# Kernel tuning notes

Measured on AMD Instinct MI355X. Metric: run time of the kernel, lower is better.

## Reference

```python
import jax, jax.numpy as jnp
import numpy as np


def setup_inputs() -> dict:
    key = jax.random.key(0)
    kq, kk, kv = jax.random.split(key, 3)
    B, H, T, D = 2, 8, 8192, 64
    return {
        "Q": jax.random.normal(kq, (B, H, T, D), dtype=jnp.float32),
        "K": jax.random.normal(kk, (B, H, T, D), dtype=jnp.float32),
        "V": jax.random.normal(kv, (B, H, T, D), dtype=jnp.float32),
        "window_size": 512,
    }


def _gather_bands(x, nb, Wn):
    # x: [B,H,T,D] -> [B,H,nb,3*Wn,D], key blocks (i-1, i, i+1) per query block i
    B, H, T, D = x.shape
    xb = x.reshape(B, H, nb, Wn, D)
    xp = jnp.pad(xb, ((0, 0), (0, 0), (1, 1), (0, 0), (0, 0)))
    return jnp.concatenate([xp[:, :, i:i + nb] for i in range(3)], axis=3)


def reference(Q, K, V, window_size):
    # Sliding-window attention: softmax over keys with |q_idx - kv_idx| <= window_size,
    # computed block-sparsely (only the 3 neighboring key blocks per query block).
    B, H, T, D = Q.shape
    Wn = int(window_size)
    assert T % Wn == 0
    nb = T // Wn
    scale = 1.0 / (D ** 0.5)

    Qb = Q.reshape(B, H, nb, Wn, D)
    Kw = _gather_bands(K, nb, Wn)  # [B,H,nb,3W,D]
    Vw = _gather_bands(V, nb, Wn)

    # scores within the band: [B,H,nb,W,3W]
    s = jnp.einsum('bhnqd,bhnkd->bhnqk', Qb, Kw) * scale

    # exact band mask: global q = n*W + q_loc, global kv = (n-1)*W + k_loc
    q_loc = jnp.arange(Wn)[:, None]
    k_loc = jnp.arange(3 * Wn)[None, :]
    band = jnp.abs(q_loc + Wn - k_loc) <= Wn          # [W, 3W]
    kv_g = (jnp.arange(nb)[:, None] - 1) * Wn + jnp.arange(3 * Wn)[None, :]  # [nb, 3W]
    valid = (kv_g >= 0) & (kv_g < T)
    mask = band[None, :, :] & valid[:, None, :]        # [nb, W, 3W]

    s = jnp.where(mask[None, None], s, -jnp.inf)
    p = jax.nn.softmax(s, axis=-1)
    o = jnp.einsum('bhnqk,bhnkd->bhnqd', p, Vw)
    return o.reshape(B, H, T, D)
```

## Files before the change

### kernel.cpp

```cpp
#include <hip/hip_runtime.h>
#include <hip/hip_bf16.h>
#include <stdint.h>

typedef __attribute__((ext_vector_type(8))) short bf16x8;
typedef __attribute__((ext_vector_type(4))) short bf16x4;
typedef __attribute__((ext_vector_type(4))) float f32x4;

#define T_SEQ   8192
#define D_HEAD  64
#define NHEADS  16
#define WIN     512
#define BQ      128
#define BK      64
#define NTILES  (T_SEQ / BK)
#define LDSR    72
#define MASKVAL (-1.0e6f)

#define WS_NEEDED ((size_t)2 * NHEADS * T_SEQ * D_HEAD * 2)

#define MFMA16(a,b,c) __builtin_amdgcn_mfma_f32_16x16x16bf16_1k(a,b,c,0,0,0)

extern "C" __device__ __attribute__((const)) float __ocml_native_exp2_f32(float);
__device__ __forceinline__ float fexp2(float x) { return __ocml_native_exp2_f32(x); }

#define GLDS16(g, l) __builtin_amdgcn_global_load_lds( \
    (const __attribute__((address_space(1))) void*)(g), \
    (__attribute__((address_space(3))) void*)(l), 16, 0, 0)

__device__ __forceinline__ short f2bf(float f) {
    union { float f; uint32_t u; } v; v.f = f;
    return (short)((v.u + 0x7FFFu + ((v.u >> 16) & 1u)) >> 16);
}

__device__ __forceinline__ uint32_t pkbf2(float lo, float hi) {
    union { __hip_bfloat162 h; uint32_t u; } c;
    c.h = __float22bfloat162_rn(make_float2(lo, hi));
    return c.u;
}

__global__ __launch_bounds__(256, 2)
void prep_kv(const float* __restrict__ Kg, const float* __restrict__ Vg,
             short* __restrict__ Kb, short* __restrict__ Vt)
{
    __shared__ float vt[64 * 65];
    const int tid  = threadIdx.x;
    const int tile = blockIdx.x & (NTILES - 1);
    const int head = blockIdx.x >> 7;
    const size_t off = ((size_t)head * T_SEQ + (size_t)tile * BK) * D_HEAD;

    const float* ks = Kg + off;
    short* kd = Kb + off;
    #pragma unroll
    for (int i = 0; i < 2; ++i) {
        int L = tid + 256 * i;
        int row = L >> 3, c = L & 7;
        const float* s = ks + row * 64 + c * 8;
        float4 a = *(const float4*)s;
        float4 b = *(const float4*)(s + 4);
        short out[8] = { f2bf(a.x), f2bf(a.y), f2bf(a.z), f2bf(a.w),
                         f2bf(b.x), f2bf(b.y), f2bf(b.z), f2bf(b.w) };
        *(bf16x8*)(kd + (row * 8 + (c ^ (row & 7))) * 8) = *(bf16x8*)out;
    }

    const float* vs = Vg + off;
    #pragma unroll
    for (int i = 0; i < 4; ++i) {
        int idx = tid + 256 * i;
        int row = idx >> 4, c4 = (idx & 15) << 2;
        float4 v = *(const float4*)(vs + row * D_HEAD + c4);
        *(float4*)&vt[row * 65 + c4] = v;
    }
    __syncthreads();
    short* vd = Vt + ((size_t)head * NTILES + tile) * (BK * D_HEAD);
    {
        int d = tid >> 2, q = tid & 3;
        #pragma unroll
        for (int h = 0; h < 2; ++h) {
            int c = h * 4 + q;
            short out[8];
            #pragma unroll
            for (int j = 0; j < 4; ++j) out[j]     = f2bf(vt[(h*32      + q*4 + j) * 65 + d]);
            #pragma unroll
            for (int j = 0; j < 4; ++j) out[4 + j] = f2bf(vt[(h*32 + 16 + q*4 + j) * 65 + d]);
            *(bf16x8*)(vd + (d * 8 + (c ^ (d & 7))) * 8) = *(bf16x8*)out;
        }
    }
}

__global__ __launch_bounds__(256, 4)
void swa_fwd(const float* __restrict__ Qg, const short* __restrict__ Kb,
             const short* __restrict__ Vt, float* __restrict__ Og)
{
    __shared__ short Ks[2][BK * D_HEAD];
    __shared__ short Vs[2][BK * D_HEAD];

    const int tid  = threadIdx.x;
    const int wave = tid >> 6;
    const int lane = tid & 63;
    const int lcol = lane & 15;
    const int quad = lane >> 4;
    const int rx   = lcol & 7;

    const int g    = blockIdx.x;
    const int head = g >> 6;
    const int qt   = ((g & 7) << 3) | ((g >> 3) & 7);
    const int q0   = qt * BQ;
    const int tq   = q0 >> 6;

    const float* Qp = Qg + (size_t)head * T_SEQ * D_HEAD;
    const short* Kp = Kb + (size_t)head * T_SEQ * D_HEAD;
    float*       Op = Og + (size_t)head * T_SEQ * D_HEAD;

    const float qscale = 0.125f * 1.44269504088896340736f;
    const int qrow_w = q0 + wave * 32;

    bf16x8 qf[2][2];
    #pragma unroll
    for (int mt = 0; mt < 2; ++mt) {
        const float* qptr = Qp + (size_t)(qrow_w + mt*16 + lcol) * D_HEAD + quad * 8;
        #pragma unroll
        for (int ks = 0; ks < 2; ++ks) {
            float4 a = *(const float4*)(qptr + ks*32);
            float4 b = *(const float4*)(qptr + ks*32 + 4);
            bf16x8 f;
            f[0]=f2bf(a.x*qscale); f[1]=f2bf(a.y*qscale); f[2]=f2bf(a.z*qscale); f[3]=f2bf(a.w*qscale);
            f[4]=f2bf(b.x*qscale); f[5]=f2bf(b.y*qscale); f[6]=f2bf(b.z*qscale); f[7]=f2bf(b.w*qscale);
            qf[mt][ks] = f;
        }
    }

    f32x4 oacc[2][4];
    f32x4 lacc[2];
    const f32x4 zero4 = {0.f, 0.f, 0.f, 0.f};
    const short oneb = (short)0x3F80;
    const bf16x4 ones4 = {oneb, oneb, oneb, oneb};
    #pragma unroll
    for (int mt = 0; mt < 2; ++mt) {
        lacc[mt] = zero4;
        #pragma unroll
        for (int nt = 0; nt < 4; ++nt) oacc[mt][nt] = zero4;
    }

    int t0 = (q0 - WIN) >> 6;            if (t0 < 0) t0 = 0;
    int t1 = (q0 + BQ - 1 + WIN) >> 6;   if (t1 > NTILES - 1) t1 = NTILES - 1;

    const int ch0 = wave * 2, ch1 = wave * 2 + 1;

    {
        const short* ksrc = Kp + (size_t)t0 * (BK * D_HEAD);
        const short* vsrc = Vt + ((size_t)head * NTILES + t0) * (BK * D_HEAD);
        GLDS16(ksrc + ch0*512 + lane*8, &Ks[0][ch0*512]);
        GLDS16(ksrc + ch1*512 + lane*8, &Ks[0][ch1*512]);
        GLDS16(vsrc + ch0*512 + lane*8, &Vs[0][ch0*512]);
        GLDS16(vsrc + ch1*512 + lane*8, &Vs[0][ch1*512]);
    }
    asm volatile("s_waitcnt vmcnt(0)" ::: "memory");
    __syncthreads();

    auto body = [&](int t, int P) {
        {
            const int tn = (t + 1 <= t1) ? t + 1 : t1;
            const short* ksrc = Kp + (size_t)tn * (BK * D_HEAD);
            const short* vsrc = Vt + ((size_t)head * NTILES + tn) * (BK * D_HEAD);
            short* kds = &Ks[P^1][0];
            short* vds = &Vs[P^1][0];
            GLDS16(ksrc + ch0*512 + lane*8, kds + ch0*512);
            GLDS16(ksrc + ch1*512 + lane*8, kds + ch1*512);
            GLDS16(vsrc + ch0*512 + lane*8, vds + ch0*512);
            GLDS16(vsrc + ch1*512 + lane*8, vds + ch1*512);
        }

        const short* Kcur = &Ks[P][0];
        const short* Vcur = &Vs[P][0];
        const bool edge = (t < tq - 6) || (t > tq + 7);

        #pragma unroll
        for (int h = 0; h < 2; ++h) {
            bf16x8 vv[4];
            #pragma unroll
            for (int nt = 0; nt < 4; ++nt)
                vv[nt] = *(const bf16x8*)&Vcur[(nt*16 + lcol)*64 + (((h*4 + quad) ^ rx) << 3)];

            f32x4 sc[2][2];
            #pragma unroll
            for (int j = 0; j < 2; ++j) { sc[j][0] = zero4; sc[j][1] = zero4; }
            #pragma unroll
            for (int ks = 0; ks < 2; ++ks) {
                #pragma unroll
                for (int j = 0; j < 2; ++j) {
                    bf16x8 kf = *(const bf16x8*)&Kcur[((2*h+j)*16 + lcol)*64
                                                      + (((ks*4 + quad) ^ rx) << 3)];
                    sc[j][0] = __builtin_amdgcn_mfma_f32_16x16x32_bf16(kf, qf[0][ks], sc[j][0], 0,0,0);
                    sc[j][1] = __builtin_amdgcn_mfma_f32_16x16x32_bf16(kf, qf[1][ks], sc[j][1], 0,0,0);
                }
            }

            if (edge) {
                #pragma unroll
                for (int j = 0; j < 2; ++j) {
                    const int kg0 = t*BK + (2*h+j)*16 + quad*4;
                    #pragma unroll
                    for (int mt = 0; mt < 2; ++mt) {
                        const int qg = qrow_w + mt*16 + lcol;
                        #pragma unroll
                        for (int r = 0; r < 4; ++r) {
                            int dq = qg - (kg0 + r);
                            if (dq > WIN || dq < -WIN) sc[j][mt][r] = MASKVAL;
                        }
                    }
                }
            }

            #pragma unroll
            for (int j = 0; j < 2; ++j) {
                bf16x4 vh[4];
                #pragma unroll
                for (int nt = 0; nt < 4; ++nt) {
                    bf16x8 v8 = vv[nt];
                    bf16x4 x = { v8[j*4+0], v8[j*4+1], v8[j*4+2], v8[j*4+3] };
                    vh[nt] = x;
                }
                #pragma unroll
                for (int mt = 0; mt < 2; ++mt) {
                    float p0 = fexp2(sc[j][mt][0]);
                    float p1 = fexp2(sc[j][mt][1]);
                    float p2 = fexp2(sc[j][mt][2]);
                    float p3 = fexp2(sc[j][mt][3]);
                    union { int2 i; bf16x4 v; } pf;
                    pf.i = make_int2((int)pkbf2(p0, p1), (int)pkbf2(p2, p3));
                    lacc[mt] = MFMA16(ones4, pf.v, lacc[mt]);
                    #pragma unroll
                    for (int nt = 0; nt < 4; ++nt)
                        oacc[mt][nt] = MFMA16(vh[nt], pf.v, oacc[mt][nt]);
                }
            }
        }

        asm volatile("s_waitcnt vmcnt(0)" ::: "memory");
        __syncthreads();
    };

    int t = t0;
    for (; t + 1 <= t1; t += 2) { body(t, 0); body(t + 1, 1); }
    if (t <= t1) body(t, 0);

    #pragma unroll
    for (int mt = 0; mt < 2; ++mt) {
        float inv = 1.0f / lacc[mt][0];
        const int qg = qrow_w + mt*16 + lcol;
        float* op = Op + (size_t)qg * D_HEAD + quad*4;
        #pragma unroll
        for (int nt = 0; nt < 4; ++nt) {
            float4 o = { oacc[mt][nt][0]*inv, oacc[mt][nt][1]*inv,
                         oacc[mt][nt][2]*inv, oacc[mt][nt][3]*inv };
            *(float4*)(op + nt*16) = o;
        }
    }
}

#define BQF     128
__global__ __launch_bounds__(256, 4)
void swa_fused_fb(const float* __restrict__ Qg, const float* __restrict__ Kg,
                  const float* __restrict__ Vg, float* __restrict__ Og)
{
    __shared__ short Ksf[BK * LDSR];
    __shared__ short Vsf[D_HEAD * LDSR];
    __shared__ float Vtmp[BK * 65];

    const int tid  = threadIdx.x;
    const int wave = tid >> 6;
    const int lane = tid & 63;
    const int lcol = lane & 15;
    const int quad = lane >> 4;

    const int g    = blockIdx.x;
    const int head = g >> 6;
    const int qt   = ((g & 7) << 3) | ((g >> 3) & 7);
    const int q0   = qt * BQF;
    const int tq   = q0 >> 6;

    const size_t hoff = (size_t)head * T_SEQ * D_HEAD;
    const float* Qp = Qg + hoff;
    const float* Kp = Kg + hoff;
    const float* Vp = Vg + hoff;
    float*       Op = Og + hoff;

    const float qscale = 0.125f * 1.44269504088896340736f;
    const int qrow_w = q0 + wave * 32;

    bf16x8 qf[2][2];
    #pragma unroll
    for (int mt = 0; mt < 2; ++mt) {
        const float* qptr = Qp + (size_t)(qrow_w + mt*16 + lcol) * D_HEAD + quad * 8;
        #pragma unroll
        for (int ks = 0; ks < 2; ++ks) {
            float4 a = *(const float4*)(qptr + ks*32);
            float4 b = *(const float4*)(qptr + ks*32 + 4);
            bf16x8 f;
            f[0]=f2bf(a.x*qscale); f[1]=f2bf(a.y*qscale); f[2]=f2bf(a.z*qscale); f[3]=f2bf(a.w*qscale);
            f[4]=f2bf(b.x*qscale); f[5]=f2bf(b.y*qscale); f[6]=f2bf(b.z*qscale); f[7]=f2bf(b.w*qscale);
            qf[mt][ks] = f;
        }
    }

    f32x4 oacc[2][4];
    float l_run[2];
    const f32x4 zero4 = {0.f, 0.f, 0.f, 0.f};
    #pragma unroll
    for (int mt = 0; mt < 2; ++mt) {
        l_run[mt] = 0.f;
        #pragma unroll
        for (int nt = 0; nt < 4; ++nt) oacc[mt][nt] = zero4;
    }

    int t0 = (q0 - WIN) >> 6;            if (t0 < 0) t0 = 0;
    int t1 = (q0 + BQF - 1 + WIN) >> 6;  if (t1 > NTILES - 1) t1 = NTILES - 1;

    const int krow0 = tid >> 3, kc = (tid & 7) << 3;
    const int krow1 = krow0 + 32;
    const int vrow  = tid >> 4, vc = (tid & 15) << 2;
    const int td    = tid >> 2, tkq = (tid & 3) << 4;

    for (int t = t0; t <= t1; ++t) {
        const float* ksrc = Kp + (size_t)t * BK * D_HEAD;
        const float* vsrc = Vp + (size_t)t * BK * D_HEAD;
        float4 k00 = *(const float4*)(ksrc + krow0*D_HEAD + kc);
        float4 k01 = *(const float4*)(ksrc + krow0*D_HEAD + kc + 4);
        float4 k10 = *(const float4*)(ksrc + krow1*D_HEAD + kc);
        float4 k11 = *(const float4*)(ksrc + krow1*D_HEAD + kc + 4);
        float4 v0  = *(const float4*)(vsrc + (vrow     )*D_HEAD + vc);
        float4 v1  = *(const float4*)(vsrc + (vrow + 16)*D_HEAD + vc);
        float4 v2  = *(const float4*)(vsrc + (vrow + 32)*D_HEAD + vc);
        float4 v3  = *(const float4*)(vsrc + (vrow + 48)*D_HEAD + vc);

        __syncthreads();

        *(float4*)&Vtmp[(vrow     )*65 + vc] = v0;
        *(float4*)&Vtmp[(vrow + 16)*65 + vc] = v1;
        *(float4*)&Vtmp[(vrow + 32)*65 + vc] = v2;
        *(float4*)&Vtmp[(vrow + 48)*65 + vc] = v3;
        *(int4*)&Ksf[krow0*LDSR + kc] = make_int4((int)pkbf2(k00.x,k00.y), (int)pkbf2(k00.z,k00.w),
                                                  (int)pkbf2(k01.x,k01.y), (int)pkbf2(k01.z,k01.w));
        *(int4*)&Ksf[krow1*LDSR + kc] = make_int4((int)pkbf2(k10.x,k10.y), (int)pkbf2(k10.z,k10.w),
                                                  (int)pkbf2(k11.x,k11.y), (int)pkbf2(k11.z,k11.w));

        __syncthreads();

        {
            uint32_t w0 = pkbf2(Vtmp[(tkq+ 0)*65 + td], Vtmp[(tkq+ 1)*65 + td]);
            uint32_t w1 = pkbf2(Vtmp[(tkq+ 2)*65 + td], Vtmp[(tkq+ 3)*65 + td]);
            uint32_t w2 = pkbf2(Vtmp[(tkq+ 4)*65 + td], Vtmp[(tkq+ 5)*65 + td]);
            uint32_t w3 = pkbf2(Vtmp[(tkq+ 6)*65 + td], Vtmp[(tkq+ 7)*65 + td]);
            uint32_t w4 = pkbf2(Vtmp[(tkq+ 8)*65 + td], Vtmp[(tkq+ 9)*65 + td]);
            uint32_t w5 = pkbf2(Vtmp[(tkq+10)*65 + td], Vtmp[(tkq+11)*65 + td]);
            uint32_t w6 = pkbf2(Vtmp[(tkq+12)*65 + td], Vtmp[(tkq+13)*65 + td]);
            uint32_t w7 = pkbf2(Vtmp[(tkq+14)*65 + td], Vtmp[(tkq+15)*65 + td]);
            *(int4*)&Vsf[td*LDSR + tkq]     = make_int4((int)w0,(int)w1,(int)w2,(int)w3);
            *(int4*)&Vsf[td*LDSR + tkq + 8] = make_int4((int)w4,(int)w5,(int)w6,(int)w7);
        }

        __syncthreads();

        const bool edge = (t < tq - 6) || (t > tq + 7);

        #pragma unroll
        for (int h = 0; h < 2; ++h) {
            f32x4 sc[2][2];
            #pragma unroll
            for (int j = 0; j < 2; ++j) { sc[j][0] = zero4; sc[j][1] = zero4; }
            #pragma unroll
            for (int ks = 0; ks < 2; ++ks) {
                #pragma unroll
                for (int j = 0; j < 2; ++j) {
                    bf16x8 kf = *(const bf16x8*)&Ksf[((2*h+j)*16 + lcol)*LDSR + ks*32 + quad*8];
                    sc[j][0] = __builtin_amdgcn_mfma_f32_16x16x32_bf16(kf, qf[0][ks], sc[j][0], 0,0,0);
                    sc[j][1] = __builtin_amdgcn_mfma_f32_16x16x32_bf16(kf, qf[1][ks], sc[j][1], 0,0,0);
                }
            }

            if (edge) {
                #pragma unroll
                for (int j = 0; j < 2; ++j) {
                    const int kg0 = t*BK + (2*h+j)*16 + quad*4;
                    #pragma unroll
                    for (int mt = 0; mt < 2; ++mt) {
                        const int qg = qrow_w + mt*16 + lcol;
                        #pragma unroll
                        for (int r = 0; r < 4; ++r) {
                            int dq = qg - (kg0 + r);
                            if (dq > WIN || dq < -WIN) sc[j][mt][r] = MASKVAL;
                        }
                    }
                }
            }

            #pragma unroll
            for (int j = 0; j < 2; ++j) {
                const int kt = 2*h + j;
                bf16x4 vf[4];
                #pragma unroll
                for (int nt = 0; nt < 4; ++nt)
                    vf[nt] = *(const bf16x4*)&Vsf[(nt*16 + lcol)*LDSR + kt*16 + quad*4];
                #pragma unroll
                for (int mt = 0; mt < 2; ++mt) {
                    float p0 = fexp2(sc[j][mt][0]);
                    float p1 = fexp2(sc[j][mt][1]);
                    float p2 = fexp2(sc[j][mt][2]);
                    float p3 = fexp2(sc[j][mt][3]);
                    l_run[mt] += (p0 + p1) + (p2 + p3);
                    union { int2 i; bf16x4 v; } pf;
                    pf.i = make_int2((int)pkbf2(p0, p1), (int)pkbf2(p2, p3));
                    #pragma unroll
                    for (int nt = 0; nt < 4; ++nt)
                        oacc[mt][nt] = MFMA16(vf[nt], pf.v, oacc[mt][nt]);
                }
            }
        }
    }

    #pragma unroll
    for (int mt = 0; mt < 2; ++mt) {
        float l = l_run[mt];
        l += __shfl_xor(l, 16, 64);
        l += __shfl_xor(l, 32, 64);
        float inv = 1.0f / l;
        const int qg = qrow_w + mt*16 + lcol;
        float* op = Op + (size_t)qg * D_HEAD + quad*4;
        #pragma unroll
        for (int nt = 0; nt < 4; ++nt) {
            float4 o = { oacc[mt][nt][0]*inv, oacc[mt][nt][1]*inv,
                         oacc[mt][nt][2]*inv, oacc[mt][nt][3]*inv };
            *(float4*)(op + nt*16) = o;
        }
    }
}

extern "C" void kernel_launch(void* const* d_in, const int* in_sizes, int n_in,
                              void* d_out, int out_size, void* d_ws, size_t ws_size,
                              hipStream_t stream)
{
    const float* Q = (const float*)d_in[0];
    const float* K = (const float*)d_in[1];
    const float* V = (const float*)d_in[2];
    float* O = (float*)d_out;

    if (ws_size >= WS_NEEDED) {
        short* Kb = (short*)d_ws;
        short* Vt = Kb + (size_t)NHEADS * T_SEQ * D_HEAD;
        prep_kv<<<dim3(NHEADS * NTILES), dim3(256), 0, stream>>>(K, V, Kb, Vt);
        swa_fwd<<<dim3(NHEADS * (T_SEQ / BQ)), dim3(256), 0, stream>>>(Q, Kb, Vt, O);
    } else {
        swa_fused_fb<<<dim3(NHEADS * (T_SEQ / BQF)), dim3(256), 0, stream>>>(Q, K, V, O);
    }
}
```

Before: 186.8 us.

## Triple-buffer K/V tiles with a single barrier and compute row sums in registers

Replaces the double-buffered K/V LDS pipeline with a three-stage ring buffer that prefetches two tiles ahead. Each iteration now waits with a partial vmcnt and a single barrier instead of a full drain at the end of the body. The MFMA-with-ones row-sum accumulation is replaced by scalar fp32 sums, reduced across quads with shuffles at the end. Shared memory grows and launch bounds drop to 3 blocks per CU, which may reduce occupancy. The row sum is now taken from unrounded fp32 probabilities rather than bf16-rounded ones.

```diff
diff --git a/kernel.cpp b/kernel.cpp
--- a/kernel.cpp
+++ b/kernel.cpp
@@ -13,6 +13,7 @@
 #define BQ      128
 #define BK      64
 #define NTILES  (T_SEQ / BK)
+#define TILE_E  (BK * D_HEAD)
 #define LDSR    72
 #define MASKVAL (-1.0e6f)
 
@@ -71,7 +72,7 @@
         *(float4*)&vt[row * 65 + c4] = v;
     }
     __syncthreads();
-    short* vd = Vt + ((size_t)head * NTILES + tile) * (BK * D_HEAD);
+    short* vd = Vt + ((size_t)head * NTILES + tile) * TILE_E;
     {
         int d = tid >> 2, q = tid & 3;
         #pragma unroll
@@ -87,12 +88,12 @@
     }
 }
 
-__global__ __launch_bounds__(256, 4)
+__global__ __launch_bounds__(256, 3)
 void swa_fwd(const float* __restrict__ Qg, const short* __restrict__ Kb,
              const short* __restrict__ Vt, float* __restrict__ Og)
 {
-    __shared__ short Ks[2][BK * D_HEAD];
-    __shared__ short Vs[2][BK * D_HEAD];
+    __shared__ short Ks[3][TILE_E];
+    __shared__ short Vs[3][TILE_E];
 
     const int tid  = threadIdx.x;
     const int wave = tid >> 6;
@@ -130,13 +131,11 @@
     }
 
     f32x4 oacc[2][4];
-    f32x4 lacc[2];
+    float l_run[2];
     const f32x4 zero4 = {0.f, 0.f, 0.f, 0.f};
-    const short oneb = (short)0x3F80;
-    const bf16x4 ones4 = {oneb, oneb, oneb, oneb};
-    #pragma unroll
-    for (int mt = 0; mt < 2; ++mt) {
-        lacc[mt] = zero4;
+    #pragma unroll
+    for (int mt = 0; mt < 2; ++mt) {
+        l_run[mt] = 0.f;
         #pragma unroll
         for (int nt = 0; nt < 4; ++nt) oacc[mt][nt] = zero4;
     }
@@ -147,31 +146,44 @@
     const int ch0 = wave * 2, ch1 = wave * 2 + 1;
 
     {
-        const short* ksrc = Kp + (size_t)t0 * (BK * D_HEAD);
-        const short* vsrc = Vt + ((size_t)head * NTILES + t0) * (BK * D_HEAD);
+        const short* ksrc = Kp + (size_t)t0 * TILE_E;
+        const short* vsrc = Vt + ((size_t)head * NTILES + t0) * TILE_E;
         GLDS16(ksrc + ch0*512 + lane*8, &Ks[0][ch0*512]);
         GLDS16(ksrc + ch1*512 + lane*8, &Ks[0][ch1*512]);
         GLDS16(vsrc + ch0*512 + lane*8, &Vs[0][ch0*512]);
         GLDS16(vsrc + ch1*512 + lane*8, &Vs[0][ch1*512]);
     }
-    asm volatile("s_waitcnt vmcnt(0)" ::: "memory");
-    __syncthreads();
-
-    auto body = [&](int t, int P) {
+    {
+        const int tn = (t0 + 1 <= t1) ? t0 + 1 : t1;
+        const short* ksrc = Kp + (size_t)tn * TILE_E;
+        const short* vsrc = Vt + ((size_t)head * NTILES + tn) * TILE_E;
+        GLDS16(ksrc + ch0*512 + lane*8, &Ks[1][ch0*512]);
+        GLDS16(ksrc + ch1*512 + lane*8, &Ks[1][ch1*512]);
+        GLDS16(vsrc + ch0*512 + lane*8, &Vs[1][ch0*512]);
+        GLDS16(vsrc + ch1*512 + lane*8, &Vs[1][ch1*512]);
+    }
+
+    int bi = 0;
+    for (int t = t0; t <= t1; ++t) {
+        asm volatile("s_waitcnt vmcnt(4)" ::: "memory");
+        __builtin_amdgcn_s_barrier();
+        asm volatile("" ::: "memory");
+
         {
-            const int tn = (t + 1 <= t1) ? t + 1 : t1;
-            const short* ksrc = Kp + (size_t)tn * (BK * D_HEAD);
-            const short* vsrc = Vt + ((size_t)head * NTILES + tn) * (BK * D_HEAD);
-            short* kds = &Ks[P^1][0];
-            short* vds = &Vs[P^1][0];
+            int tn = t + 2; if (tn > t1) tn = t1;
+            int bw = bi + 2; if (bw >= 3) bw -= 3;
+            const short* ksrc = Kp + (size_t)tn * TILE_E;
+            const short* vsrc = Vt + ((size_t)head * NTILES + tn) * TILE_E;
+            short* kds = &Ks[bw][0];
+            short* vds = &Vs[bw][0];
             GLDS16(ksrc + ch0*512 + lane*8, kds + ch0*512);
             GLDS16(ksrc + ch1*512 + lane*8, kds + ch1*512);
             GLDS16(vsrc + ch0*512 + lane*8, vds + ch0*512);
             GLDS16(vsrc + ch1*512 + lane*8, vds + ch1*512);
         }
 
-        const short* Kcur = &Ks[P][0];
-        const short* Vcur = &Vs[P][0];
+        const short* Kcur = &Ks[bi][0];
+        const short* Vcur = &Vs[bi][0];
         const bool edge = (t < tq - 6) || (t > tq + 7);
 
         #pragma unroll
@@ -226,9 +238,9 @@
                     float p1 = fexp2(sc[j][mt][1]);
                     float p2 = fexp2(sc[j][mt][2]);
                     float p3 = fexp2(sc[j][mt][3]);
+                    l_run[mt] += (p0 + p1) + (p2 + p3);
                     union { int2 i; bf16x4 v; } pf;
                     pf.i = make_int2((int)pkbf2(p0, p1), (int)pkbf2(p2, p3));
-                    lacc[mt] = MFMA16(ones4, pf.v, lacc[mt]);
                     #pragma unroll
                     for (int nt = 0; nt < 4; ++nt)
                         oacc[mt][nt] = MFMA16(vh[nt], pf.v, oacc[mt][nt]);
@@ -236,17 +248,17 @@
             }
         }
 
-        asm volatile("s_waitcnt vmcnt(0)" ::: "memory");
-        __syncthreads();
-    };
-
-    int t = t0;
-    for (; t + 1 <= t1; t += 2) { body(t, 0); body(t + 1, 1); }
-    if (t <= t1) body(t, 0);
-
-    #pragma unroll
-    for (int mt = 0; mt < 2; ++mt) {
-        float inv = 1.0f / lacc[mt][0];
+        bi = (bi == 2) ? 0 : bi + 1;
+    }
+
+    asm volatile("s_waitcnt vmcnt(0)" ::: "memory");
+
+    #pragma unroll
+    for (int mt = 0; mt < 2; ++mt) {
+        float l = l_run[mt];
+        l += __shfl_xor(l, 16, 64);
+        l += __shfl_xor(l, 32, 64);
+        float inv = 1.0f / l;
         const int qg = qrow_w + mt*16 + lcol;
         float* op = Op + (size_t)qg * D_HEAD + quad*4;
         #pragma unroll
```

After: 187.9 us. Within noise of the previous version (+0.5%).
